# Kernel optimization log

Measured on AMD Instinct MI355X. Metric: run time of the kernel, lower is better.

## Reference

```python
import jax, jax.numpy as jnp
import numpy as np

N_EMBD = 768
HEAD_SIZE = 64

def setup_inputs() -> dict:
    key = jax.random.key(0)
    k1, k2, k3, k4 = jax.random.split(key, 4)
    B, T = 8, 2048
    x = jax.random.normal(k1, (B, T, N_EMBD), dtype=jnp.float32)
    s = 1.0 / np.sqrt(N_EMBD)
    Wk = jax.random.normal(k2, (N_EMBD, HEAD_SIZE), dtype=jnp.float32) * s
    Wq = jax.random.normal(k3, (N_EMBD, HEAD_SIZE), dtype=jnp.float32) * s
    Wv = jax.random.normal(k4, (N_EMBD, HEAD_SIZE), dtype=jnp.float32) * s
    return {"x": x, "Wk": Wk, "Wq": Wq, "Wv": Wv}

def reference(x, Wk, Wq, Wv):
    # x: [B, T, C]; projections: [B, T, H]
    B, T, C = x.shape
    k = jnp.einsum('btc,ch->bth', x, Wk)
    q = jnp.einsum('btc,ch->bth', x, Wq)
    v = jnp.einsum('btc,ch->bth', x, Wv)
    # scores [B, T, T], scaled by head_size^-0.5
    wei = jnp.einsum('bth,bsh->bts', q, k) * (HEAD_SIZE ** -0.5)
    causal = jnp.tril(jnp.ones((T, T), dtype=bool))
    wei = jnp.where(causal, wei, -jnp.inf)
    wei = jax.nn.softmax(wei, axis=-1)
    # dropout omitted (eval mode / deterministic reference)
    out = jnp.einsum('bts,bsh->bth', wei, v)
    return out
```

## Files before the change

### kernel.cpp

```cpp
#include <hip/hip_runtime.h>

#define B_ 8
#define T_ 2048
#define C_ 768
#define H_ 64
#define QT_ (T_ / 64)
#define NCH_ 8

typedef __bf16 bf16x8 __attribute__((ext_vector_type(8)));
typedef unsigned short ushort8 __attribute__((ext_vector_type(8)));
typedef float f32x4 __attribute__((ext_vector_type(4)));
typedef float f32x16 __attribute__((ext_vector_type(16)));

typedef __attribute__((address_space(1))) const void g_void;
typedef __attribute__((address_space(3))) void lds_void;

static __device__ __forceinline__ unsigned short f32_to_bf16(float f) {
  unsigned int u = __float_as_uint(f);
  u += 0x7FFFu + ((u >> 16) & 1u);
  return (unsigned short)(u >> 16);
}

static __device__ __forceinline__ float bf16_to_f32(unsigned short u) {
  return __uint_as_float(((unsigned int)u) << 16);
}

static __device__ __forceinline__ unsigned int cvtpk_bf16(float a, float b) {
  unsigned int r;
  asm("v_cvt_pk_bf16_f32 %0, %1, %2" : "=v"(r) : "v"(a), "v"(b));
  return r;
}

static __device__ __forceinline__ f32x4 mfma16(ushort8 a, ushort8 b, f32x4 c) {
  return __builtin_amdgcn_mfma_f32_16x16x32_bf16(
      __builtin_bit_cast(bf16x8, a), __builtin_bit_cast(bf16x8, b), c, 0, 0, 0);
}

static __device__ __forceinline__ f32x16 mfma32(ushort8 a, ushort8 b, f32x16 c) {
  return __builtin_amdgcn_mfma_f32_32x32x16_bf16(
      __builtin_bit_cast(bf16x8, a), __builtin_bit_cast(bf16x8, b), c, 0, 0, 0);
}

template <int BASE>
static __device__ __forceinline__ ushort8 packA(const f32x16& p) {
  unsigned int a1 = cvtpk_bf16(p[BASE + 0], p[BASE + 1]);
  unsigned int a2 = cvtpk_bf16(p[BASE + 2], p[BASE + 3]);
  unsigned int a3 = cvtpk_bf16(p[BASE + 4], p[BASE + 5]);
  unsigned int a4 = cvtpk_bf16(p[BASE + 6], p[BASE + 7]);
  asm("v_permlane32_swap_b32 %0, %1" : "+v"(a1), "+v"(a3));
  asm("v_permlane32_swap_b32 %0, %1" : "+v"(a2), "+v"(a4));
  uint4 w = {a1, a2, a3, a4};
  return __builtin_bit_cast(ushort8, w);
}

__global__ void prep_w_kernel(const float* __restrict__ Wk, const float* __restrict__ Wq,
                              const float* __restrict__ Wv, unsigned short* __restrict__ Wt) {
  int g = blockIdx.x * 256 + threadIdx.x;
  if (g >= 24 * 768) return;
  int ks = g / 768, s = g - ks * 768;
  int n = s >> 2, perm = s & 3;
  int k8 = perm ^ (n & 3) ^ ((n >> 2) & 3);
  int p = n >> 6, col = n & 63;
  const float* W = (p == 0) ? Wk : (p == 1) ? Wq : Wv;
  float sc = (p == 1) ? 0.125f * 1.44269504088896f : 1.0f;
  int kbase = ks * 32 + k8 * 8;
  ushort8 v;
#pragma unroll
  for (int e = 0; e < 8; ++e) v[e] = f32_to_bf16(W[(kbase + e) * 64 + col] * sc);
  *(ushort8*)(Wt + (size_t)g * 8) = v;
}

__global__ __launch_bounds__(512) void proj_kernel(
    const float* __restrict__ x, const unsigned short* __restrict__ Wt,
    unsigned short* __restrict__ Qf, unsigned short* __restrict__ Kf,
    unsigned short* __restrict__ Vf) {
  __shared__ unsigned short Wl[2][6144];
  __shared__ unsigned short Xl[2][1024];
  const int tid = threadIdx.x;
  const int wave = tid >> 6, lane = tid & 63;
  const int lo = lane & 15, hi = lane >> 4;
  const int rg = wave & 1, ch3 = wave >> 1;
  const int row0 = blockIdx.x * 32;

  f32x4 acc[3];
#pragma unroll
  for (int t = 0; t < 3; ++t) acc[t] = (f32x4){0.f, 0.f, 0.f, 0.f};

  const int xr = (tid & 127) >> 2;
  const int xk8 = tid & 3;
  const int xslot = xr * 4 + (xk8 ^ (xr & 3) ^ ((xr >> 2) & 3));
  const float* xsrc = x + (size_t)(row0 + xr) * C_ + xk8 * 8;

  const int arow = rg * 16 + lo;
  const int aaddr = (arow * 4 + (hi ^ (arow & 3) ^ ((arow >> 2) & 3))) * 8;

  auto wstage = [&](int buf, int ks) {
    const unsigned short* base = Wt + (size_t)ks * 6144 + lane * 8;
    for (int is = wave; is < 12; is += 8)
      __builtin_amdgcn_global_load_lds((g_void*)(base + is * 512),
          (lds_void*)(&Wl[buf][is * 512]), 16, 0, 0);
  };

  float4 xa0 = {}, xa1 = {}, xb0 = {}, xb1 = {};

  wstage(0, 0);
  if (tid < 128) {
    xa0 = *(const float4*)(xsrc);
    xa1 = *(const float4*)(xsrc + 4);
  }

  for (int ks = 0; ks < 24; ++ks) {
    const int cur = ks & 1;
    asm volatile("s_waitcnt vmcnt(0)" ::: "memory");
    __syncthreads();
    if (ks + 1 < 24) {
      wstage(cur ^ 1, ks + 1);
      if (tid < 128) {
        xb0 = *(const float4*)(xsrc + (ks + 1) * 32);
        xb1 = *(const float4*)(xsrc + (ks + 1) * 32 + 4);
      }
    }
    if (tid < 128) {
      unsigned int dd[4];
      dd[0] = cvtpk_bf16(xa0.x, xa0.y);
      dd[1] = cvtpk_bf16(xa0.z, xa0.w);
      dd[2] = cvtpk_bf16(xa1.x, xa1.y);
      dd[3] = cvtpk_bf16(xa1.z, xa1.w);
      *(uint4*)(&Xl[cur][xslot * 8]) = *(uint4*)dd;
    }
    __syncthreads();
    ushort8 af = *(const ushort8*)(&Xl[cur][aaddr]);
#pragma unroll
    for (int t = 0; t < 3; ++t) {
      const int n = ch3 * 48 + t * 16 + lo;
      const int baddr = (n * 4 + (hi ^ (n & 3) ^ ((n >> 2) & 3))) * 8;
      ushort8 bfr = *(const ushort8*)(&Wl[cur][baddr]);
      acc[t] = mfma16(af, bfr, acc[t]);
    }
    xa0 = xb0; xa1 = xb1;
  }

#pragma unroll
  for (int t = 0; t < 3; ++t) {
    const int n = ch3 * 48 + t * 16 + lo;
    const int p = n >> 6, d = n & 63;
#pragma unroll
    for (int r = 0; r < 4; ++r) {
      const int rgl = row0 + rg * 16 + hi * 4 + r;
      const int b = rgl >> 11;
      const int tt = rgl & (T_ - 1);
      unsigned short val = f32_to_bf16(acc[t][r]);
      if (p == 2) {
        const size_t addr = ((((size_t)b * 128 + (tt >> 4)) * 2 + (d >> 5)) * 64 +
                             ((tt >> 3) & 1) * 32 + (d & 31)) * 8 + (tt & 7);
        Vf[addr] = val;
      } else {
        const size_t addr = ((((size_t)b * 64 + (tt >> 5)) * 4 + (d >> 4)) * 64 +
                             ((d >> 3) & 1) * 32 + (tt & 31)) * 8 + (d & 7);
        if (p == 0) Kf[addr] = val; else Qf[addr] = val;
      }
    }
  }
}

__global__ __launch_bounds__(128) void attn_part_kernel(
    const unsigned short* __restrict__ Qf, const unsigned short* __restrict__ Kf,
    const unsigned short* __restrict__ Vf, unsigned short* __restrict__ Opb,
    float* __restrict__ Ml) {
  const int qt = blockIdx.x;
  const int b = blockIdx.y;
  const int ch = blockIdx.z;
  const int t0 = ch * 4;
  if (t0 > qt) return;
  const int t1 = min(qt, t0 + 3);

  const int tid = threadIdx.x;
  const int wave = tid >> 6;
  const int lane = tid & 63;
  const int il = lane & 31;
  const int h = lane >> 5;
  const int i0w = qt * 64 + wave * 32;

  const unsigned short* qbase = Qf + ((((size_t)b * 64 + (qt * 2 + wave)) * 4) << 9) + lane * 8;
  const unsigned short* kbase = Kf + (((size_t)b * 64) << 11) + lane * 8;
  const unsigned short* vbase = Vf + (((size_t)b * 128) << 10) + lane * 8;

  ushort8 qf[4];
#pragma unroll
  for (int dc = 0; dc < 4; ++dc) qf[dc] = *(const ushort8*)(qbase + (dc << 9));

  f32x16 o0 = {}, o1 = {};
  float m = -1e30f, lsum = 0.f;

  for (int jt = t0; jt <= t1; ++jt) {
    const int j0 = jt * 64;
    const size_t jg = (size_t)(jt * 2);

    ushort8 kf0[4], kf1[4];
#pragma unroll
    for (int dc = 0; dc < 4; ++dc) {
      kf0[dc] = *(const ushort8*)(kbase + (jg << 11) + (dc << 9));
      kf1[dc] = *(const ushort8*)(kbase + ((jg + 1) << 11) + (dc << 9));
    }
    ushort8 vf0[4], vf1[4];
#pragma unroll
    for (int c = 0; c < 4; ++c) {
      const size_t jc = (size_t)(jt * 4 + c);
      vf0[c] = *(const ushort8*)(vbase + (jc << 10));
      vf1[c] = *(const ushort8*)(vbase + (jc << 10) + (1 << 9));
    }

    f32x16 s0 = {}, s1 = {};
    __builtin_amdgcn_s_setprio(1);
#pragma unroll
    for (int dc = 0; dc < 4; ++dc) {
      s0 = mfma32(kf0[dc], qf[dc], s0);
      s1 = mfma32(kf1[dc], qf[dc], s1);
    }
    __builtin_amdgcn_s_setprio(0);

    if (jt == qt) {
      const int ig = i0w + il;
#pragma unroll
      for (int r = 0; r < 16; ++r) {
        const int jl = j0 + (r & 3) + 8 * (r >> 2) + 4 * h;
        if (jl > ig) s0[r] = -1e30f;
        if (jl + 32 > ig) s1[r] = -1e30f;
      }
    }

    float mx[8];
#pragma unroll
    for (int r = 0; r < 8; ++r) mx[r] = fmaxf(fmaxf(s0[r], s0[r + 8]), fmaxf(s1[r], s1[r + 8]));
#pragma unroll
    for (int d = 4; d >= 1; d >>= 1)
#pragma unroll
      for (int r = 0; r < d; ++r) mx[r] = fmaxf(mx[r], mx[r + d]);
    float tm = fmaxf(mx[0], __shfl_xor(mx[0], 32));
    const float mnew = fmaxf(m, tm);
    const float scl = exp2f(m - mnew);
    m = mnew;
    float sa = 0.f, sb = 0.f, sc2 = 0.f, sd = 0.f;
#pragma unroll
    for (int r = 0; r < 16; r += 4) {
      s0[r] = exp2f(s0[r] - mnew);     sa += s0[r];
      s0[r + 1] = exp2f(s0[r + 1] - mnew); sb += s0[r + 1];
      s0[r + 2] = exp2f(s0[r + 2] - mnew); sc2 += s0[r + 2];
      s0[r + 3] = exp2f(s0[r + 3] - mnew); sd += s0[r + 3];
    }
#pragma unroll
    for (int r = 0; r < 16; r += 4) {
      s1[r] = exp2f(s1[r] - mnew);     sa += s1[r];
      s1[r + 1] = exp2f(s1[r + 1] - mnew); sb += s1[r + 1];
      s1[r + 2] = exp2f(s1[r + 2] - mnew); sc2 += s1[r + 2];
      s1[r + 3] = exp2f(s1[r + 3] - mnew); sd += s1[r + 3];
    }
    float ts = (sa + sb) + (sc2 + sd);
    ts += __shfl_xor(ts, 32);
    lsum = lsum * scl + ts;
    o0 *= scl;
    o1 *= scl;

    __builtin_amdgcn_s_setprio(1);
#pragma unroll
    for (int c = 0; c < 4; ++c) {
      ushort8 pa = (c == 0) ? packA<0>(s0) : (c == 1) ? packA<8>(s0)
                 : (c == 2) ? packA<0>(s1) : packA<8>(s1);
      o0 = mfma32(vf0[c], pa, o0);
      o1 = mfma32(vf1[c], pa, o1);
    }
    __builtin_amdgcn_s_setprio(0);
  }

  const size_t pb = (size_t)(b * QT_ + qt) * NCH_ + ch;
  unsigned short* op = Opb + pb * 4096 + (size_t)(wave * 32 + il) * 64;
#pragma unroll
  for (int g = 0; g < 4; ++g) {
    unsigned int w0[2], w1[2];
    w0[0] = cvtpk_bf16(o0[4 * g + 0], o0[4 * g + 1]);
    w0[1] = cvtpk_bf16(o0[4 * g + 2], o0[4 * g + 3]);
    w1[0] = cvtpk_bf16(o1[4 * g + 0], o1[4 * g + 1]);
    w1[1] = cvtpk_bf16(o1[4 * g + 2], o1[4 * g + 3]);
    *(uint2*)(op + 8 * g + 4 * h) = *(uint2*)w0;
    *(uint2*)(op + 32 + 8 * g + 4 * h) = *(uint2*)w1;
  }
  if (h == 0) {
    float* ml = Ml + pb * 128;
    ml[wave * 32 + il] = m;
    ml[64 + wave * 32 + il] = lsum;
  }
}

__global__ __launch_bounds__(256) void attn_comb_kernel(
    const unsigned short* __restrict__ Opb, const float* __restrict__ Ml,
    float* __restrict__ out) {
  const int qt = blockIdx.x;
  const int b = blockIdx.y;
  const int nc = (qt >> 2) + 1;
  const int row = threadIdx.x >> 2;
  const int c0 = (threadIdx.x & 3) * 16;
  const size_t pbase = (size_t)(b * QT_ + qt) * NCH_;

  float m_g = -1e30f;
  for (int c = 0; c < nc; ++c) m_g = fmaxf(m_g, Ml[(pbase + c) * 128 + row]);
  float l_g = 0.f;
  for (int c = 0; c < nc; ++c)
    l_g += Ml[(pbase + c) * 128 + 64 + row] * exp2f(Ml[(pbase + c) * 128 + row] - m_g);
  const float inv = 1.0f / l_g;

  f32x4 a0 = {0,0,0,0}, a1 = {0,0,0,0}, a2 = {0,0,0,0}, a3 = {0,0,0,0};
  for (int c = 0; c < nc; ++c) {
    const float wc = exp2f(Ml[(pbase + c) * 128 + row] - m_g);
    const unsigned short* op = Opb + (pbase + c) * 4096 + row * 64 + c0;
    ushort8 u0 = *(const ushort8*)(op);
    ushort8 u1 = *(const ushort8*)(op + 8);
    a0 += (f32x4){bf16_to_f32(u0[0]), bf16_to_f32(u0[1]), bf16_to_f32(u0[2]), bf16_to_f32(u0[3])} * wc;
    a1 += (f32x4){bf16_to_f32(u0[4]), bf16_to_f32(u0[5]), bf16_to_f32(u0[6]), bf16_to_f32(u0[7])} * wc;
    a2 += (f32x4){bf16_to_f32(u1[0]), bf16_to_f32(u1[1]), bf16_to_f32(u1[2]), bf16_to_f32(u1[3])} * wc;
    a3 += (f32x4){bf16_to_f32(u1[4]), bf16_to_f32(u1[5]), bf16_to_f32(u1[6]), bf16_to_f32(u1[7])} * wc;
  }
  float* o = out + ((size_t)b * T_ + qt * 64 + row) * 64 + c0;
  *(f32x4*)(o) = a0 * inv;
  *(f32x4*)(o + 4) = a1 * inv;
  *(f32x4*)(o + 8) = a2 * inv;
  *(f32x4*)(o + 12) = a3 * inv;
}

extern "C" void kernel_launch(void* const* d_in, const int* in_sizes, int n_in,
                              void* d_out, int out_size, void* d_ws, size_t ws_size,
                              hipStream_t stream) {
  const float* x = (const float*)d_in[0];
  const float* Wk = (const float*)d_in[1];
  const float* Wq = (const float*)d_in[2];
  const float* Wv = (const float*)d_in[3];
  float* out = (float*)d_out;

  char* ws = (char*)d_ws;
  unsigned short* Qf = (unsigned short*)(ws);
  unsigned short* Kf = (unsigned short*)(ws + (2u << 20));
  unsigned short* Vf = (unsigned short*)(ws + (4u << 20));
  unsigned short* Wt = (unsigned short*)(ws + (6u << 20));
  unsigned short* Opb = (unsigned short*)(ws + (8u << 20));
  float* Ml = (float*)(ws + (24u << 20));

  prep_w_kernel<<<dim3(72), dim3(256), 0, stream>>>(Wk, Wq, Wv, Wt);
  proj_kernel<<<dim3((B_ * T_) / 32), dim3(512), 0, stream>>>(x, Wt, Qf, Kf, Vf);
  attn_part_kernel<<<dim3(QT_, B_, NCH_), dim3(128), 0, stream>>>(Qf, Kf, Vf, Opb, Ml);
  attn_comb_kernel<<<dim3(QT_, B_), dim3(256), 0, stream>>>(Opb, Ml, out);
}
```

Measured before the change: 59.68 us.

## Load x fragments directly into registers and add lazy softmax rescaling

The projection kernel now has every wave load its own x fragment from global memory and convert it in registers. This removes the x LDS staging buffer and one barrier per step, and it processes K in 64-wide steps using a larger W LDS buffer. The attention kernel skips updating the running max and rescaling the output accumulators unless some lane's tile max exceeds the current max by more than 8 in log2 units. Skipping the rescale is meant to save exp and multiply work, but it lets exponentials grow up to 2^8 before rescaling, which carries a small precision risk.

```diff
diff --git a/kernel.cpp b/kernel.cpp
--- a/kernel.cpp
+++ b/kernel.cpp
@@ -74,75 +74,70 @@
     const float* __restrict__ x, const unsigned short* __restrict__ Wt,
     unsigned short* __restrict__ Qf, unsigned short* __restrict__ Kf,
     unsigned short* __restrict__ Vf) {
-  __shared__ unsigned short Wl[2][6144];
-  __shared__ unsigned short Xl[2][1024];
+  __shared__ unsigned short Wl[2][12288];
   const int tid = threadIdx.x;
   const int wave = tid >> 6, lane = tid & 63;
   const int lo = lane & 15, hi = lane >> 4;
-  const int rg = wave & 1, ch3 = wave >> 1;
+  const int rg = wave & 1, cq = wave >> 1;
   const int row0 = blockIdx.x * 32;
 
   f32x4 acc[3];
 #pragma unroll
   for (int t = 0; t < 3; ++t) acc[t] = (f32x4){0.f, 0.f, 0.f, 0.f};
 
-  const int xr = (tid & 127) >> 2;
-  const int xk8 = tid & 3;
-  const int xslot = xr * 4 + (xk8 ^ (xr & 3) ^ ((xr >> 2) & 3));
-  const float* xsrc = x + (size_t)(row0 + xr) * C_ + xk8 * 8;
-
-  const int arow = rg * 16 + lo;
-  const int aaddr = (arow * 4 + (hi ^ (arow & 3) ^ ((arow >> 2) & 3))) * 8;
-
-  auto wstage = [&](int buf, int ks) {
-    const unsigned short* base = Wt + (size_t)ks * 6144 + lane * 8;
-    for (int is = wave; is < 12; is += 8)
-      __builtin_amdgcn_global_load_lds((g_void*)(base + is * 512),
-          (lds_void*)(&Wl[buf][is * 512]), 16, 0, 0);
+  const float* xrow = x + (size_t)(row0 + rg * 16 + lo) * C_ + hi * 8;
+
+  auto wstage = [&](int buf, int ks64) {
+    const unsigned short* src = Wt + (size_t)ks64 * 12288 + wave * 512 + lane * 8;
+#pragma unroll
+    for (int is = 0; is < 3; ++is)
+      __builtin_amdgcn_global_load_lds((g_void*)(src + is * 4096),
+          (lds_void*)(&Wl[buf][is * 4096 + wave * 512]), 16, 0, 0);
   };
 
-  float4 xa0 = {}, xa1 = {}, xb0 = {}, xb1 = {};
-
+  float4 xa[4], xb[4];
   wstage(0, 0);
-  if (tid < 128) {
-    xa0 = *(const float4*)(xsrc);
-    xa1 = *(const float4*)(xsrc + 4);
-  }
-
-  for (int ks = 0; ks < 24; ++ks) {
+#pragma unroll
+  for (int c = 0; c < 2; ++c) {
+    xa[2 * c] = *(const float4*)(xrow + c * 32);
+    xa[2 * c + 1] = *(const float4*)(xrow + c * 32 + 4);
+  }
+
+  for (int ks = 0; ks < 12; ++ks) {
     const int cur = ks & 1;
     asm volatile("s_waitcnt vmcnt(0)" ::: "memory");
     __syncthreads();
-    if (ks + 1 < 24) {
+    if (ks + 1 < 12) {
       wstage(cur ^ 1, ks + 1);
-      if (tid < 128) {
-        xb0 = *(const float4*)(xsrc + (ks + 1) * 32);
-        xb1 = *(const float4*)(xsrc + (ks + 1) * 32 + 4);
+#pragma unroll
+      for (int c = 0; c < 2; ++c) {
+        xb[2 * c] = *(const float4*)(xrow + (ks + 1) * 64 + c * 32);
+        xb[2 * c + 1] = *(const float4*)(xrow + (ks + 1) * 64 + c * 32 + 4);
       }
     }
-    if (tid < 128) {
+#pragma unroll
+    for (int c = 0; c < 2; ++c) {
       unsigned int dd[4];
-      dd[0] = cvtpk_bf16(xa0.x, xa0.y);
-      dd[1] = cvtpk_bf16(xa0.z, xa0.w);
-      dd[2] = cvtpk_bf16(xa1.x, xa1.y);
-      dd[3] = cvtpk_bf16(xa1.z, xa1.w);
-      *(uint4*)(&Xl[cur][xslot * 8]) = *(uint4*)dd;
-    }
-    __syncthreads();
-    ushort8 af = *(const ushort8*)(&Xl[cur][aaddr]);
-#pragma unroll
-    for (int t = 0; t < 3; ++t) {
-      const int n = ch3 * 48 + t * 16 + lo;
-      const int baddr = (n * 4 + (hi ^ (n & 3) ^ ((n >> 2) & 3))) * 8;
-      ushort8 bfr = *(const ushort8*)(&Wl[cur][baddr]);
-      acc[t] = mfma16(af, bfr, acc[t]);
-    }
-    xa0 = xb0; xa1 = xb1;
+      dd[0] = cvtpk_bf16(xa[2 * c].x, xa[2 * c].y);
+      dd[1] = cvtpk_bf16(xa[2 * c].z, xa[2 * c].w);
+      dd[2] = cvtpk_bf16(xa[2 * c + 1].x, xa[2 * c + 1].y);
+      dd[3] = cvtpk_bf16(xa[2 * c + 1].z, xa[2 * c + 1].w);
+      ushort8 af = __builtin_bit_cast(ushort8, *(uint4*)dd);
+#pragma unroll
+      for (int t = 0; t < 3; ++t) {
+        const int n = (cq * 3 + t) * 16 + lo;
+        const int baddr = c * 6144 + (n * 4 + (hi ^ (n & 3) ^ ((n >> 2) & 3))) * 8;
+        ushort8 bfr = *(const ushort8*)(&Wl[cur][baddr]);
+        acc[t] = mfma16(af, bfr, acc[t]);
+      }
+    }
+#pragma unroll
+    for (int q = 0; q < 4; ++q) xa[q] = xb[q];
   }
 
 #pragma unroll
   for (int t = 0; t < 3; ++t) {
-    const int n = ch3 * 48 + t * 16 + lo;
+    const int n = (cq * 3 + t) * 16 + lo;
     const int p = n >> 6, d = n & 63;
 #pragma unroll
     for (int r = 0; r < 4; ++r) {
@@ -237,29 +232,32 @@
 #pragma unroll
       for (int r = 0; r < d; ++r) mx[r] = fmaxf(mx[r], mx[r + d]);
     float tm = fmaxf(mx[0], __shfl_xor(mx[0], 32));
-    const float mnew = fmaxf(m, tm);
-    const float scl = exp2f(m - mnew);
-    m = mnew;
+    float scl = 1.0f;
+    if (!__all(tm <= m + 8.0f)) {
+      const float mnew = fmaxf(m, tm);
+      scl = exp2f(m - mnew);
+      m = mnew;
+      o0 *= scl;
+      o1 *= scl;
+    }
     float sa = 0.f, sb = 0.f, sc2 = 0.f, sd = 0.f;
 #pragma unroll
     for (int r = 0; r < 16; r += 4) {
-      s0[r] = exp2f(s0[r] - mnew);     sa += s0[r];
-      s0[r + 1] = exp2f(s0[r + 1] - mnew); sb += s0[r + 1];
-      s0[r + 2] = exp2f(s0[r + 2] - mnew); sc2 += s0[r + 2];
-      s0[r + 3] = exp2f(s0[r + 3] - mnew); sd += s0[r + 3];
+      s0[r] = exp2f(s0[r] - m);     sa += s0[r];
+      s0[r + 1] = exp2f(s0[r + 1] - m); sb += s0[r + 1];
+      s0[r + 2] = exp2f(s0[r + 2] - m); sc2 += s0[r + 2];
+      s0[r + 3] = exp2f(s0[r + 3] - m); sd += s0[r + 3];
     }
 #pragma unroll
     for (int r = 0; r < 16; r += 4) {
-      s1[r] = exp2f(s1[r] - mnew);     sa += s1[r];
-      s1[r + 1] = exp2f(s1[r + 1] - mnew); sb += s1[r + 1];
-      s1[r + 2] = exp2f(s1[r + 2] - mnew); sc2 += s1[r + 2];
-      s1[r + 3] = exp2f(s1[r + 3] - mnew); sd += s1[r + 3];
+      s1[r] = exp2f(s1[r] - m);     sa += s1[r];
+      s1[r + 1] = exp2f(s1[r + 1] - m); sb += s1[r + 1];
+      s1[r + 2] = exp2f(s1[r + 2] - m); sc2 += s1[r + 2];
+      s1[r + 3] = exp2f(s1[r + 3] - m); sd += s1[r + 3];
     }
     float ts = (sa + sb) + (sc2 + sd);
     ts += __shfl_xor(ts, 32);
     lsum = lsum * scl + ts;
-    o0 *= scl;
-    o1 *= scl;
 
     __builtin_amdgcn_s_setprio(1);
 #pragma unroll
```

After: 70.08 us. +17.4%, slower.
